# Optimization experiments

Measured on AMD Instinct MI355X. Metric: run time of the kernel, lower is better.

The kernel has to match this reference:

```python
import jax, jax.numpy as jnp
import numpy as np

NUE, NAP, E = 512, 1024, 524288
D, OC, HID, PH = 4, 64, 32, 4  # raw feat dim, out_channels, out//2, power hid


def _lin(key, fi, fo):
    k1, k2 = jax.random.split(key)
    s = 1.0 / np.sqrt(fi)
    W = jax.random.uniform(k1, (fi, fo), minval=-s, maxval=s, dtype=jnp.float32)
    b = jax.random.uniform(k2, (fo,), minval=-s, maxval=s, dtype=jnp.float32)
    return W, b


_LAYER_SPECS = [
    ("c1_msg", D + D, HID), ("c1_upd", HID + D, OC - D), ("c1_ew", 3 * D, OC - D),
    ("c2_msg", OC + D, HID), ("c2_upd", HID + D, OC - D), ("c2_ew", D + OC + D, OC - D),
    ("c3u_msg", 2 * OC, HID), ("c3u_upd", HID + OC, OC - D), ("c3u_ew", 3 * OC, OC - D),
    ("c3d_msg", 2 * OC, HID), ("c3d_upd", HID + OC, OC - D), ("c3d_ew", 3 * OC, OC - D),
    ("pe1", OC, PH), ("pe2", PH, 1),
]


def setup_inputs() -> dict:
    key = jax.random.key(0)
    ks = jax.random.split(key, 24)
    inp = {}
    inp["x_ue"] = jax.random.normal(ks[0], (NUE, D), dtype=jnp.float32)
    inp["x_ap"] = jax.random.normal(ks[1], (NAP, D), dtype=jnp.float32)
    inp["ea_up"] = jax.random.normal(ks[2], (E, D), dtype=jnp.float32)
    inp["ea_down"] = jax.random.normal(ks[3], (E, D), dtype=jnp.float32)
    inp["ei_up_src"] = jax.random.randint(ks[4], (E,), 0, NUE, dtype=jnp.int32)
    inp["ei_up_dst"] = jax.random.randint(ks[5], (E,), 0, NAP, dtype=jnp.int32)
    inp["ei_down_src"] = jax.random.randint(ks[6], (E,), 0, NAP, dtype=jnp.int32)
    inp["ei_down_dst"] = jax.random.randint(ks[7], (E,), 0, NUE, dtype=jnp.int32)
    for i, (n, fi, fo) in enumerate(_LAYER_SPECS):
        W, b = _lin(ks[8 + i], fi, fo)
        inp[n + "_W"] = W
        inp[n + "_b"] = b
    inp["pe_ln_g"] = jnp.ones((PH,), dtype=jnp.float32)
    inp["pe_ln_b"] = jnp.zeros((PH,), dtype=jnp.float32)
    return inp


def _lrelu(x):
    return jnp.where(x >= 0, x, 0.1 * x)


def _mlp1(x, W, b):  # one MLP block: Linear -> LeakyReLU(0.1) (dropout = eval identity)
    return _lrelu(x @ W + b)


def _conv_step(x_src, x_dst, ea, src_idx, dst_idx, n_dst,
               msg_W, msg_b, upd_W, upd_b, ew_W, ew_b, residual):
    xj = x_src[src_idx]                                   # [E, d_src] gather
    m = _mlp1(jnp.concatenate([xj, ea], axis=1), msg_W, msg_b)  # [E, HID]
    agg = jax.ops.segment_sum(m, dst_idx, num_segments=n_dst)   # scatter-add -> [n_dst, HID]
    tmp = _mlp1(jnp.concatenate([x_dst, agg], axis=1), upd_W, upd_b)  # [n_dst, OC-D]
    if residual:
        tmp = tmp + x_dst[:, D:]
    new_x_dst = jnp.concatenate([x_dst[:, :D], tmp], axis=1)     # [n_dst, OC]
    xi = x_dst[dst_idx]                                   # old x_dst per torch code
    e = _mlp1(jnp.concatenate([xj, ea, xi], axis=1), ew_W, ew_b)  # [E, OC-D]
    new_ea = jnp.concatenate([ea[:, :D], e], axis=1)             # [E, OC]
    return new_x_dst, new_ea


def _layernorm(x, g, b, eps=1e-5):
    mu = jnp.mean(x, axis=-1, keepdims=True)
    var = jnp.mean(jnp.square(x - mu), axis=-1, keepdims=True)
    return (x - mu) * jax.lax.rsqrt(var + eps) * g + b


def reference(x_ue, x_ap, ea_up, ea_down,
              ei_up_src, ei_up_dst, ei_down_src, ei_down_dst,
              c1_msg_W, c1_msg_b, c1_upd_W, c1_upd_b, c1_ew_W, c1_ew_b,
              c2_msg_W, c2_msg_b, c2_upd_W, c2_upd_b, c2_ew_W, c2_ew_b,
              c3u_msg_W, c3u_msg_b, c3u_upd_W, c3u_upd_b, c3u_ew_W, c3u_ew_b,
              c3d_msg_W, c3d_msg_b, c3d_upd_W, c3d_upd_b, c3d_ew_W, c3d_ew_b,
              pe1_W, pe1_b, pe2_W, pe2_b, pe_ln_g, pe_ln_b):
    # conv1: UE --up--> AP
    x_ap, ea_up = _conv_step(x_ue, x_ap, ea_up, ei_up_src, ei_up_dst, NAP,
                             c1_msg_W, c1_msg_b, c1_upd_W, c1_upd_b, c1_ew_W, c1_ew_b, False)
    # conv2: AP --down--> UE
    x_ue, ea_down = _conv_step(x_ap, x_ue, ea_down, ei_down_src, ei_down_dst, NUE,
                               c2_msg_W, c2_msg_b, c2_upd_W, c2_upd_b, c2_ew_W, c2_ew_b, False)
    # conv3 handles both edge types (residual since src_dim == out_channels)
    x_ap, ea_up = _conv_step(x_ue, x_ap, ea_up, ei_up_src, ei_up_dst, NAP,
                             c3u_msg_W, c3u_msg_b, c3u_upd_W, c3u_upd_b, c3u_ew_W, c3u_ew_b, True)
    x_ue, ea_down = _conv_step(x_ap, x_ue, ea_down, ei_down_src, ei_down_dst, NUE,
                               c3d_msg_W, c3d_msg_b, c3d_upd_W, c3d_upd_b, c3d_ew_W, c3d_ew_b, True)
    # power head on down edges: Lin -> LayerNorm -> LeakyReLU -> Lin
    h = _lrelu(_layernorm(ea_down @ pe1_W + pe1_b, pe_ln_g, pe_ln_b))
    power = h @ pe2_W + pe2_b                                   # [E, 1]
    ea_down = jnp.concatenate([ea_down[:, :D], power], axis=1)  # [E, D+1]
    return (x_ue, x_ap, ea_up, ea_down)
```

## Files before the change

kernel.cpp:

```cpp
#include <hip/hip_runtime.h>

typedef __attribute__((ext_vector_type(8))) short bf16x8;
typedef __attribute__((ext_vector_type(4))) float f32x4;

static constexpr int EN   = 524288;
static constexpr int NUE_ = 512;
static constexpr int NAP_ = 1024;
static constexpr int HID_ = 32;
static constexpr int OD_  = 60;
static constexpr int OC_  = 64;
static constexpr int NB_  = 256;
static constexpr int CH_  = EN / NB_;

__device__ __forceinline__ unsigned short f2bf(float x) {
  unsigned int u = __float_as_uint(x);
  return (unsigned short)((u + 0x7fffu + ((u >> 16) & 1u)) >> 16);
}
__device__ __forceinline__ float bf2f(unsigned int u) {
  return __uint_as_float(u << 16);
}

__global__ __launch_bounds__(256)
void lhist2x(const int* __restrict__ up_dst, const int* __restrict__ dn_dst,
             int* __restrict__ bh_up, int* __restrict__ bh_dn,
             unsigned short* __restrict__ lr_up, unsigned short* __restrict__ lr_dn,
             const float* __restrict__ c3u_ew, const float* __restrict__ c3u_msg,
             const float* __restrict__ c3d_ew, const float* __restrict__ c3d_msg,
             unsigned short* __restrict__ we3u, unsigned short* __restrict__ wm3u,
             unsigned short* __restrict__ we3d, unsigned short* __restrict__ wm3d,
             const float* __restrict__ x_ue, const float* __restrict__ x_ap,
             const float* __restrict__ c1_ew, const float* __restrict__ c1_msg,
             const float* __restrict__ c1_ew_b, const float* __restrict__ c1_msg_b,
             const float* __restrict__ c2_ew, const float* __restrict__ c2_ew_b,
             float* __restrict__ Y1j, float* __restrict__ Y1i,
             float* __restrict__ Y1m, float* __restrict__ Y2i)
{
  __shared__ int h[NAP_];
  const int t = threadIdx.x;
  if (blockIdx.x >= 2 * NB_) {
    const int xb = blockIdx.x - 2 * NB_;
    if (xb < 48) {
      const float* W; unsigned short* out; int NREAL, NPAD, i;
      if (xb < 16)      { W = c3u_ew;  out = we3u; NREAL = 60; NPAD = 64; i = xb * 256 + t; }
      else if (xb < 24) { W = c3u_msg; out = wm3u; NREAL = 32; NPAD = 32; i = (xb - 16) * 256 + t; }
      else if (xb < 40) { W = c3d_ew;  out = we3d; NREAL = 60; NPAD = 64; i = (xb - 24) * 256 + t; }
      else              { W = c3d_msg; out = wm3d; NREAL = 32; NPAD = 32; i = (xb - 40) * 256 + t; }
      if (i >= NPAD * 64) return;
      int n = i >> 6, k = i & 63;
      float v = (n < NREAL) ? W[(size_t)(64 + k) * NREAL + n] : 0.f;
      out[i] = f2bf(v);
    } else {
      const int tid = (xb - 48) * 256 + t;
      if (tid < NUE_) {
        const float4 x = *reinterpret_cast<const float4*>(x_ue + (size_t)tid * 4);
        const float xv[4] = {x.x, x.y, x.z, x.w};
        for (int o = 0; o < OD_; ++o) {
          float a = 0.f, bb = c2_ew_b[o];
          #pragma unroll
          for (int k = 0; k < 4; ++k) {
            a = fmaf(xv[k], c1_ew[k * OD_ + o], a);
            bb = fmaf(xv[k], c2_ew[(68 + k) * OD_ + o], bb);
          }
          Y1j[(size_t)tid * OD_ + o] = a;
          Y2i[(size_t)tid * OD_ + o] = bb;
        }
        for (int o = 0; o < HID_; ++o) {
          float m = c1_msg_b[o];
          #pragma unroll
          for (int k = 0; k < 4; ++k) m = fmaf(xv[k], c1_msg[k * HID_ + o], m);
          Y1m[(size_t)tid * HID_ + o] = m;
        }
      } else if (tid < NUE_ + NAP_) {
        const int r = tid - NUE_;
        const float4 x = *reinterpret_cast<const float4*>(x_ap + (size_t)r * 4);
        const float xv[4] = {x.x, x.y, x.z, x.w};
        for (int o = 0; o < OD_; ++o) {
          float a = c1_ew_b[o];
          #pragma unroll
          for (int k = 0; k < 4; ++k) a = fmaf(xv[k], c1_ew[(8 + k) * OD_ + o], a);
          Y1i[(size_t)r * OD_ + o] = a;
        }
      }
    }
    return;
  }
  const bool up = blockIdx.x < NB_;
  const int b = up ? blockIdx.x : blockIdx.x - NB_;
  const int NBINS = up ? NAP_ : NUE_;
  const int* dst = up ? up_dst : dn_dst;
  int* bh = up ? bh_up : bh_dn;
  unsigned short* lrank = up ? lr_up : lr_dn;
  for (int i = t; i < NBINS; i += 256) h[i] = 0;
  __syncthreads();
  const int base = b * CH_;
  #pragma unroll 1
  for (int i = t; i < CH_; i += 256)
    lrank[base + i] = (unsigned short)atomicAdd(&h[dst[base + i]], 1);
  __syncthreads();
  for (int i = t; i < NBINS; i += 256)
    bh[(size_t)i * NB_ + b] = h[i];
}

__global__ __launch_bounds__(64)
void bscanA2(int* __restrict__ bh_up, int* __restrict__ bh_dn,
             int* __restrict__ bs_up, int* __restrict__ bs_dn)
{
  const bool up = blockIdx.x < NAP_;
  const int bin = up ? blockIdx.x : blockIdx.x - NAP_;
  int* bh = up ? bh_up : bh_dn;
  int* binsum = up ? bs_up : bs_dn;
  const int l = threadIdx.x;
  int4 v = *reinterpret_cast<int4*>(&bh[(size_t)bin * NB_ + l * 4]);
  const int s0 = v.x, s1 = s0 + v.y, s2 = s1 + v.z, s3 = s2 + v.w;
  int inc = s3;
  #pragma unroll
  for (int d2 = 1; d2 < 64; d2 <<= 1) {
    int n = __shfl_up(inc, d2, 64);
    if (l >= d2) inc += n;
  }
  const int exc = inc - s3;
  int4 o; o.x = exc; o.y = exc + s0; o.z = exc + s1; o.w = exc + s2;
  *reinterpret_cast<int4*>(&bh[(size_t)bin * NB_ + l * 4]) = o;
  if (l == 63) binsum[bin] = inc;
}

__global__ __launch_bounds__(256)
void bscanB2(const int* __restrict__ bs_up, int* __restrict__ off_up,
             const int* __restrict__ bs_dn, int* __restrict__ off_dn)
{
  const bool up = blockIdx.x == 0;
  const int NBINS = up ? NAP_ : NUE_;
  const int K = NBINS / 256;
  const int* binsum = up ? bs_up : bs_dn;
  int* off = up ? off_up : off_dn;
  __shared__ int wtot[4];
  const int t = threadIdx.x, lane = t & 63, wid = t >> 6;
  int loc[4]; int s = 0;
  for (int k = 0; k < K; ++k) { loc[k] = binsum[t * K + k]; s += loc[k]; }
  int inc = s;
  #pragma unroll
  for (int d2 = 1; d2 < 64; d2 <<= 1) {
    int n = __shfl_up(inc, d2, 64);
    if (lane >= d2) inc += n;
  }
  if (lane == 63) wtot[wid] = inc;
  __syncthreads();
  int woff = 0;
  #pragma unroll
  for (int ww = 0; ww < 4; ++ww) if (ww < wid) woff += wtot[ww];
  int a = woff + inc - s;
  for (int k = 0; k < K; ++k) { off[t * K + k] = a; a += loc[k]; }
  if (t == 255) off[NBINS] = a;
}

__global__ __launch_bounds__(256)
void rankc2(const int* __restrict__ up_dst, const int* __restrict__ up_src,
            const int* __restrict__ dn_dst, const int* __restrict__ dn_src,
            const unsigned short* __restrict__ lr_up, const unsigned short* __restrict__ lr_dn,
            const int* __restrict__ bh_up, const int* __restrict__ bh_dn,
            const int* __restrict__ off_up, const int* __restrict__ off_dn,
            int* __restrict__ rank_dn,
            int* __restrict__ perm_up, int* __restrict__ srcP_up, int* __restrict__ dstP_up,
            int* __restrict__ perm_dn, int* __restrict__ srcP_dn, int* __restrict__ dstP_dn)
{
  const int gid = blockIdx.x * 256 + threadIdx.x;
  const bool up = gid < EN;
  const int e = up ? gid : gid - EN;
  const int* dst = up ? up_dst : dn_dst;
  const int* src = up ? up_src : dn_src;
  const unsigned short* lrank = up ? lr_up : lr_dn;
  const int* bh = up ? bh_up : bh_dn;
  const int* off = up ? off_up : off_dn;
  const int blk = e / CH_;
  const int d = dst[e];
  const int rk = off[d] + bh[(size_t)d * NB_ + blk] + (int)lrank[e];
  if (up) {
    perm_up[rk] = e; srcP_up[rk] = src[e]; dstP_up[rk] = d;
  } else {
    rank_dn[e] = rk;
    perm_dn[rk] = e; srcP_dn[rk] = src[e]; dstP_dn[rk] = d;
  }
}

__global__ __launch_bounds__(256)
void e12n(const float* __restrict__ ea_in,
          const int* __restrict__ perm, const int* __restrict__ srcP,
          const int* __restrict__ off,
          const float* __restrict__ Yje, const float* __restrict__ Yie,
          const float* __restrict__ Ym,
          const float* __restrict__ We,
          const float* __restrict__ Wm,
          unsigned short* __restrict__ outB,
          const float* __restrict__ x_in,
          const float* __restrict__ W, const float* __restrict__ b,
          float* __restrict__ x_out,
          const float* __restrict__ WtA, float* __restrict__ YA,
          const float* __restrict__ WtB, const float* __restrict__ bB, float* __restrict__ YB,
          const float* __restrict__ WtC, const float* __restrict__ bC, float* __restrict__ YC)
{
  __shared__ unsigned short Eb[64 * 72];
  __shared__ float RedF[64][33];
  __shared__ float Part[8][33];
  __shared__ float Ag[32];
  __shared__ float Xr[4];
  __shared__ float Xn[OC_];
  const int d = blockIdx.x, t = threadIdx.x;
  const int beg = off[d], end = off[d + 1];
  const int r = t >> 2, j = t & 3;
  const int c0 = j * 15, m0 = j * 8;
  if (t < 4) Xr[t] = x_in[(size_t)d * 4 + t];
  float yie[15];
  #pragma unroll
  for (int c = 0; c < 15; ++c) yie[c] = Yie[(size_t)d * OD_ + c0 + c];
  float am[8] = {0.f, 0.f, 0.f, 0.f, 0.f, 0.f, 0.f, 0.f};

  for (int sb = beg; sb < end; sb += 64) {
    const int slot = sb + r;
    const bool act = slot < end;
    const int e = act ? perm[slot] : 0;
    const int s = act ? srcP[slot] : 0;
    float4 ea = act ? *reinterpret_cast<const float4*>(ea_in + (size_t)e * 4)
                    : make_float4(0.f, 0.f, 0.f, 0.f);
    const float eav[4] = {ea.x, ea.y, ea.z, ea.w};
    float acc[15];
    #pragma unroll
    for (int c = 0; c < 15; ++c) acc[c] = Yje[(size_t)s * OD_ + c0 + c] + yie[c];
    #pragma unroll
    for (int k = 0; k < 4; ++k)
      #pragma unroll
      for (int c = 0; c < 15; ++c)
        acc[c] = fmaf(eav[k], We[k * OD_ + c0 + c], acc[c]);
    if (act) {
      #pragma unroll
      for (int c = 0; c < 15; ++c) {
        float v = acc[c] >= 0.f ? acc[c] : 0.1f * acc[c];
        Eb[r * 72 + 4 + c0 + c] = f2bf(v);
      }
      if (j == 0) {
        Eb[r * 72 + 0] = f2bf(ea.x); Eb[r * 72 + 1] = f2bf(ea.y);
        Eb[r * 72 + 2] = f2bf(ea.z); Eb[r * 72 + 3] = f2bf(ea.w);
      }
    }
    float m[8];
    #pragma unroll
    for (int c = 0; c < 8; ++c) m[c] = Ym[(size_t)s * HID_ + m0 + c];
    #pragma unroll
    for (int k = 0; k < 4; ++k)
      #pragma unroll
      for (int c = 0; c < 8; ++c)
        m[c] = fmaf(eav[k], Wm[k * HID_ + m0 + c], m[c]);
    if (act) {
      #pragma unroll
      for (int c = 0; c < 8; ++c)
        am[c] += m[c] >= 0.f ? m[c] : 0.1f * m[c];
    }
    __syncthreads();
    const int nact = end - sb < 64 ? end - sb : 64;
    for (int idx = t; idx < nact * 8; idx += 256) {
      int row = idx >> 3, ch = idx & 7;
      *reinterpret_cast<uint4*>(outB + (size_t)(sb + row) * OC_ + ch * 8) =
          *reinterpret_cast<const uint4*>(&Eb[row * 72 + ch * 8]);
    }
    __syncthreads();
  }
  #pragma unroll
  for (int c = 0; c < 8; ++c) RedF[r][m0 + c] = am[c];
  __syncthreads();
  {
    const int col = t & 31, g = t >> 5;
    float s = 0.f;
    #pragma unroll
    for (int r2 = 0; r2 < 8; ++r2) s += RedF[g * 8 + r2][col];
    Part[g][col] = s;
  }
  __syncthreads();
  if (t < 32) {
    float s = 0.f;
    #pragma unroll
    for (int g2 = 0; g2 < 8; ++g2) s += Part[g2][t];
    Ag[t] = s;
  }
  __syncthreads();
  if (t < OD_) {
    float acc = b[t];
    #pragma unroll
    for (int k = 0; k < 4; ++k) acc = fmaf(Xr[k], W[k * OD_ + t], acc);
    #pragma unroll 4
    for (int k = 0; k < HID_; ++k) acc = fmaf(Ag[k], W[(4 + k) * OD_ + t], acc);
    acc = acc >= 0.f ? acc : 0.1f * acc;
    x_out[(size_t)d * OC_ + 4 + t] = acc;
    Xn[4 + t] = acc;
  } else if (t < OC_) {
    x_out[(size_t)d * OC_ + (t - OD_)] = Xr[t - OD_];
    Xn[t - OD_] = Xr[t - OD_];
  }
  __syncthreads();
  if (t < OD_) {
    float a = 0.f;
    #pragma unroll 4
    for (int k = 0; k < OC_; ++k) a = fmaf(Xn[k], WtA[k * OD_ + t], a);
    YA[(size_t)d * OD_ + t] = a;
  } else if (t >= 64 && t < 96) {
    const int cc = t - 64;
    float a = bB[cc];
    #pragma unroll 4
    for (int k = 0; k < OC_; ++k) a = fmaf(Xn[k], WtB[k * HID_ + cc], a);
    YB[(size_t)d * HID_ + cc] = a;
  } else if (t >= 128 && t < 188) {
    const int cc = t - 128;
    float a = bC[cc];
    #pragma unroll 4
    for (int k = 0; k < OC_; ++k) a = fmaf(Xn[k], WtC[k * OD_ + cc], a);
    YC[(size_t)d * OD_ + cc] = a;
  }
}

template<bool FUSE>
__global__ __launch_bounds__(256)
void edge3(const unsigned short* __restrict__ eaB,
           const float* __restrict__ ea0_src,
           const int* __restrict__ perm,
           const int* __restrict__ srcP, const int* __restrict__ dstP,
           const unsigned short* __restrict__ Wet, const unsigned short* __restrict__ Wmt,
           const float* __restrict__ Yje, const float* __restrict__ Yie,
           const float* __restrict__ Ym,
           float* __restrict__ agg,
           float* __restrict__ ea_out,
           float* __restrict__ pT,
           const float* __restrict__ pe1_W)
{
  const int t = threadIdx.x, l = t & 63, w = t >> 6;
  const int lr = l & 15, lkb = l >> 4;
  const int sW = blockIdx.x * 256 + w * 64;

  bf16x8 be[4][2], bm[2][2];
  #pragma unroll
  for (int nt = 0; nt < 4; ++nt)
    #pragma unroll
    for (int kk = 0; kk < 2; ++kk)
      be[nt][kk] = *reinterpret_cast<const bf16x8*>(Wet + (nt * 16 + lr) * 64 + kk * 32 + lkb * 8);
  #pragma unroll
  for (int nt = 0; nt < 2; ++nt)
    #pragma unroll
    for (int kk = 0; kk < 2; ++kk)
      bm[nt][kk] = *reinterpret_cast<const bf16x8*>(Wmt + (nt * 16 + lr) * 64 + kk * 32 + lkb * 8);

  float accLo = 0.f, accHi = 0.f;
  int curD = -1;

  #pragma unroll 1
  for (int tile = 0; tile < 4; ++tile) {
    const int s0t = sW + tile * 16;
    const unsigned short* ar = eaB + (size_t)(s0t + lr) * OC_ + lkb * 8;
    bf16x8 a[2];
    a[0] = *reinterpret_cast<const bf16x8*>(ar);
    a[1] = *reinterpret_cast<const bf16x8*>(ar + 32);

    f32x4 accE[4] = {f32x4{0,0,0,0}, f32x4{0,0,0,0}, f32x4{0,0,0,0}, f32x4{0,0,0,0}};
    f32x4 accM[2] = {f32x4{0,0,0,0}, f32x4{0,0,0,0}};
    #pragma unroll
    for (int kk = 0; kk < 2; ++kk) {
      #pragma unroll
      for (int nt = 0; nt < 4; ++nt)
        accE[nt] = __builtin_amdgcn_mfma_f32_16x16x32_bf16(a[kk], be[nt][kk], accE[nt], 0, 0, 0);
      #pragma unroll
      for (int nt = 0; nt < 2; ++nt)
        accM[nt] = __builtin_amdgcn_mfma_f32_16x16x32_bf16(a[kk], bm[nt][kk], accM[nt], 0, 0, 0);
    }
    #pragma unroll
    for (int r = 0; r < 4; ++r) {
      const int sl = s0t + lkb * 4 + r;
      const int s = srcP[sl], d = dstP[sl];
      float v0 = accM[0][r] + Ym[(size_t)s * HID_ + lr];
      float v1 = accM[1][r] + Ym[(size_t)s * HID_ + 16 + lr];
      v0 = v0 >= 0.f ? v0 : 0.1f * v0;
      v1 = v1 >= 0.f ? v1 : 0.1f * v1;
      const int q0 = (2 * lr) & 15, q1 = (2 * lr + 1) & 15;
      float t00 = __shfl(v0, q0, 16), t10 = __shfl(v1, q0, 16);
      float t01 = __shfl(v0, q1, 16), t11 = __shfl(v1, q1, 16);
      float lo = (lr < 8) ? t00 : t10;
      float hi = (lr < 8) ? t01 : t11;
      if (d != curD) {
        if (curD >= 0) {
          atomicAdd(&agg[(size_t)curD * HID_ + 2 * lr], accLo);
          atomicAdd(&agg[(size_t)curD * HID_ + 2 * lr + 1], accHi);
        }
        curD = d; accLo = lo; accHi = hi;
      } else {
        accLo += lo; accHi += hi;
      }

      float val[4];
      #pragma unroll
      for (int nt = 0; nt < 4; ++nt) {
        int col = nt * 16 + lr;
        float v = (col < OD_)
            ? accE[nt][r] + Yje[(size_t)s * OD_ + col] + Yie[(size_t)d * OD_ + col]
            : 0.f;
        val[nt] = v >= 0.f ? v : 0.1f * v;
      }
      if constexpr (!FUSE) {
        const int e = perm[sl];
        #pragma unroll
        for (int nt = 0; nt < 4; ++nt) {
          int col = nt * 16 + lr;
          if (col < OD_) ea_out[(size_t)e * OC_ + 4 + col] = val[nt];
        }
        if (lr == 0) {
          float4 ea0 = *reinterpret_cast<const float4*>(ea0_src + (size_t)e * 4);
          *reinterpret_cast<float4*>(ea_out + (size_t)e * OC_) = ea0;
        }
      } else {
        float p4[4] = {0.f, 0.f, 0.f, 0.f};
        #pragma unroll
        for (int nt = 0; nt < 4; ++nt) {
          int col = nt * 16 + lr;
          if (col < OD_) {
            #pragma unroll
            for (int jj = 0; jj < 4; ++jj)
              p4[jj] = fmaf(val[nt], pe1_W[(4 + col) * 4 + jj], p4[jj]);
          }
        }
        #pragma unroll
        for (int mk = 1; mk < 16; mk <<= 1) {
          #pragma unroll
          for (int jj = 0; jj < 4; ++jj)
            p4[jj] += __shfl_xor(p4[jj], mk, 64);
        }
        if (lr == 0)
          *reinterpret_cast<float4*>(pT + (size_t)sl * 4) =
              make_float4(p4[0], p4[1], p4[2], p4[3]);
      }
    }
  }
  if (curD >= 0) {
    atomicAdd(&agg[(size_t)curD * HID_ + 2 * lr], accLo);
    atomicAdd(&agg[(size_t)curD * HID_ + 2 * lr + 1], accHi);
  }
}

template<int LX, bool RES>
__device__ __forceinline__
void nodeup_body(int d, int t,
                 const float* __restrict__ x_in,
                 const float* __restrict__ agg,
                 const float* __restrict__ W, const float* __restrict__ b,
                 float* __restrict__ x_out,
                 const float* WtA, float* YA,
                 const float* WtB, const float* bB, float* YB)
{
  __shared__ float Ag[32];
  __shared__ float Xr[LX];
  __shared__ float Xn[OC_];
  if (t < 32) Ag[t] = agg[(size_t)d * HID_ + t];
  if (t < LX) Xr[t] = x_in[(size_t)d * LX + t];
  __syncthreads();
  if (t < OD_) {
    float acc = b[t];
    #pragma unroll 4
    for (int k = 0; k < LX; ++k) acc = fmaf(Xr[k], W[k * OD_ + t], acc);
    #pragma unroll 4
    for (int k = 0; k < HID_; ++k) acc = fmaf(Ag[k], W[(LX + k) * OD_ + t], acc);
    acc = acc >= 0.f ? acc : 0.1f * acc;
    if constexpr (RES) acc += Xr[4 + t];
    x_out[(size_t)d * OC_ + 4 + t] = acc;
    Xn[4 + t] = acc;
  } else if (t < OC_) {
    x_out[(size_t)d * OC_ + (t - OD_)] = Xr[t - OD_];
    Xn[t - OD_] = Xr[t - OD_];
  }
  if (WtA == nullptr) return;
  __syncthreads();
  if (t < OD_) {
    float a = 0.f;
    #pragma unroll 4
    for (int k = 0; k < OC_; ++k) a = fmaf(Xn[k], WtA[k * OD_ + t], a);
    YA[(size_t)d * OD_ + t] = a;
  } else if (t >= 64 && t < 96) {
    const int cc = t - 64;
    float a = bB[cc];
    #pragma unroll 4
    for (int k = 0; k < OC_; ++k) a = fmaf(Xn[k], WtB[k * HID_ + cc], a);
    YB[(size_t)d * HID_ + cc] = a;
  }
}

template<int LX, bool RES>
__global__ __launch_bounds__(256)
void nodeupT(const float* __restrict__ x_in, const float* __restrict__ agg,
             const float* __restrict__ W, const float* __restrict__ b,
             float* __restrict__ x_out,
             const float* WtA, float* YA,
             const float* WtB, const float* bB, float* YB)
{
  nodeup_body<LX, RES>(blockIdx.x, threadIdx.x, x_in, agg, W, b, x_out,
                       WtA, YA, WtB, bB, YB);
}

__global__ __launch_bounds__(256)
void nodeup_pow(const float* __restrict__ x_in, const float* __restrict__ agg,
                const float* __restrict__ W, const float* __restrict__ b,
                float* __restrict__ x_out,
                const float* __restrict__ ea0_src, const int* __restrict__ rank,
                const float* __restrict__ pT,
                const float* __restrict__ pe1_W, const float* __restrict__ pe1_b,
                const float* __restrict__ pe2_W, const float* __restrict__ pe2_b,
                const float* __restrict__ ln_g, const float* __restrict__ ln_b,
                float* __restrict__ outp)
{
  if (blockIdx.x < NUE_) {
    nodeup_body<OC_, true>(blockIdx.x, threadIdx.x, x_in, agg, W, b, x_out,
                           nullptr, nullptr, nullptr, nullptr, nullptr);
    return;
  }
  const int e = (blockIdx.x - NUE_) * 256 + threadIdx.x;
  const int rk = rank[e];
  const float4 p4 = *reinterpret_cast<const float4*>(pT + (size_t)rk * 4);
  const float4 ea0 = *reinterpret_cast<const float4*>(ea0_src + (size_t)e * 4);
  const float pv[4] = {p4.x, p4.y, p4.z, p4.w};
  float v4[4];
  #pragma unroll
  for (int jj = 0; jj < 4; ++jj)
    v4[jj] = pv[jj] + pe1_b[jj]
           + ea0.x * pe1_W[0 * 4 + jj] + ea0.y * pe1_W[1 * 4 + jj]
           + ea0.z * pe1_W[2 * 4 + jj] + ea0.w * pe1_W[3 * 4 + jj];
  const float mu = 0.25f * (v4[0] + v4[1] + v4[2] + v4[3]);
  float var = 0.f;
  #pragma unroll
  for (int jj = 0; jj < 4; ++jj) { float dd = v4[jj] - mu; var = fmaf(dd, dd, var); }
  var *= 0.25f;
  const float rstd = rsqrtf(var + 1e-5f);
  float p = pe2_b[0];
  #pragma unroll
  for (int jj = 0; jj < 4; ++jj) {
    float h = (v4[jj] - mu) * rstd * ln_g[jj] + ln_b[jj];
    h = h >= 0.f ? h : 0.1f * h;
    p = fmaf(h, pe2_W[jj], p);
  }
  float* orow = outp + (size_t)e * 5;
  orow[0] = ea0.x; orow[1] = ea0.y; orow[2] = ea0.z; orow[3] = ea0.w;
  orow[4] = p;
}

extern "C" void kernel_launch(void* const* d_in, const int* in_sizes, int n_in,
                              void* d_out, int out_size, void* d_ws, size_t ws_size,
                              hipStream_t stream)
{
  const float* x_ue    = (const float*)d_in[0];
  const float* x_ap    = (const float*)d_in[1];
  const float* ea_up   = (const float*)d_in[2];
  const float* ea_down = (const float*)d_in[3];
  const int* up_src = (const int*)d_in[4];
  const int* up_dst = (const int*)d_in[5];
  const int* dn_src = (const int*)d_in[6];
  const int* dn_dst = (const int*)d_in[7];
  const float* c1_msg_W = (const float*)d_in[8];  const float* c1_msg_b = (const float*)d_in[9];
  const float* c1_upd_W = (const float*)d_in[10]; const float* c1_upd_b = (const float*)d_in[11];
  const float* c1_ew_W  = (const float*)d_in[12]; const float* c1_ew_b  = (const float*)d_in[13];
  const float* c2_msg_W = (const float*)d_in[14]; const float* c2_msg_b = (const float*)d_in[15];
  const float* c2_upd_W = (const float*)d_in[16]; const float* c2_upd_b = (const float*)d_in[17];
  const float* c2_ew_W  = (const float*)d_in[18]; const float* c2_ew_b  = (const float*)d_in[19];
  const float* c3u_msg_W= (const float*)d_in[20]; const float* c3u_msg_b= (const float*)d_in[21];
  const float* c3u_upd_W= (const float*)d_in[22]; const float* c3u_upd_b= (const float*)d_in[23];
  const float* c3u_ew_W = (const float*)d_in[24]; const float* c3u_ew_b = (const float*)d_in[25];
  const float* c3d_msg_W= (const float*)d_in[26]; const float* c3d_msg_b= (const float*)d_in[27];
  const float* c3d_upd_W= (const float*)d_in[28]; const float* c3d_upd_b= (const float*)d_in[29];
  const float* c3d_ew_W = (const float*)d_in[30]; const float* c3d_ew_b = (const float*)d_in[31];
  const float* pe1_W = (const float*)d_in[32]; const float* pe1_b = (const float*)d_in[33];
  const float* pe2_W = (const float*)d_in[34]; const float* pe2_b = (const float*)d_in[35];
  const float* ln_g  = (const float*)d_in[36]; const float* ln_b  = (const float*)d_in[37];

  float* out    = (float*)d_out;
  float* x_ue_o = out;
  float* x_ap_o = out + (size_t)NUE_ * OC_;
  float* ea_up_o = x_ap_o + (size_t)NAP_ * OC_;
  float* ea_dn_o = ea_up_o + (size_t)EN * OC_;

  float* agg3 = (float*)d_ws;
  float* agg4 = agg3 + NAP_ * HID_;
  int* ip = (int*)(agg4 + NUE_ * HID_);
  int* rank_dn = ip; ip += EN;
  int* perm_up = ip; ip += EN;
  int* src_upP = ip; ip += EN;
  int* dst_upP = ip; ip += EN;
  int* perm_dn = ip; ip += EN;
  int* src_dnP = ip; ip += EN;
  int* dst_dnP = ip; ip += EN;
  int* bh_up   = ip; ip += NAP_ * NB_;
  int* bh_dn   = ip; ip += NUE_ * NB_;
  int* off_up  = ip; ip += NAP_ + 1;
  int* off_dn  = ip; ip += NUE_ + 1;
  int* bs_up   = ip; ip += NAP_;
  int* bs_dn   = ip; ip += NUE_;
  unsigned short* lr_up = (unsigned short*)ip; ip += EN / 2;
  unsigned short* lr_dn = (unsigned short*)ip; ip += EN / 2;
  float* p = (float*)ip;
  float* Y1j = p;  p += NUE_ * OD_;  float* Y1i = p; p += NAP_ * OD_;  float* Y1m = p; p += NUE_ * HID_;
  float* Y2j = p;  p += NAP_ * OD_;  float* Y2i = p; p += NUE_ * OD_;  float* Y2m = p; p += NAP_ * HID_;
  float* Y3uj = p; p += NUE_ * OD_;  float* Y3ui = p; p += NAP_ * OD_; float* Y3um = p; p += NUE_ * HID_;
  float* Y3dj = p; p += NAP_ * OD_;  float* Y3di = p; p += NUE_ * OD_; float* Y3dm = p; p += NAP_ * HID_;
  float* pT = p;   p += (size_t)EN * 4;
  unsigned short* us = (unsigned short*)p;
  unsigned short* ea_up_bf = us;  us += (size_t)EN * OC_;
  unsigned short* ea_dn_bf = us;  us += (size_t)EN * OC_;
  unsigned short* we3u = us; us += 64 * 64;
  unsigned short* wm3u = us; us += 32 * 64;
  unsigned short* we3d = us; us += 64 * 64;
  unsigned short* wm3d = us; us += 32 * 64;

  hipMemsetAsync(agg3, 0, sizeof(float) * (NAP_ + NUE_) * HID_, stream);

  const dim3 blk(256);
  const dim3 ege(EN / 256);

  lhist2x<<<dim3(2 * NB_ + 56), blk, 0, stream>>>(
      up_dst, dn_dst, bh_up, bh_dn, lr_up, lr_dn,
      c3u_ew_W, c3u_msg_W, c3d_ew_W, c3d_msg_W, we3u, wm3u, we3d, wm3d,
      x_ue, x_ap, c1_ew_W, c1_msg_W, c1_ew_b, c1_msg_b, c2_ew_W, c2_ew_b,
      Y1j, Y1i, Y1m, Y2i);
  bscanA2<<<dim3(NAP_ + NUE_), dim3(64), 0, stream>>>(bh_up, bh_dn, bs_up, bs_dn);
  bscanB2<<<dim3(2), blk, 0, stream>>>(bs_up, off_up, bs_dn, off_dn);
  rankc2<<<dim3(2 * EN / 256), blk, 0, stream>>>(
      up_dst, up_src, dn_dst, dn_src, lr_up, lr_dn, bh_up, bh_dn, off_up, off_dn,
      rank_dn, perm_up, src_upP, dst_upP, perm_dn, src_dnP, dst_dnP);

  e12n<<<dim3(NAP_), blk, 0, stream>>>(
      ea_up, perm_up, src_upP, off_up, Y1j, Y1i, Y1m,
      c1_ew_W + 4 * OD_, c1_msg_W + 4 * HID_, ea_up_bf,
      x_ap, c1_upd_W, c1_upd_b, x_ap_o,
      c2_ew_W, Y2j, c2_msg_W, c2_msg_b, Y2m,
      c3u_ew_W + 128 * OD_, c3u_ew_b, Y3ui);

  e12n<<<dim3(NUE_), blk, 0, stream>>>(
      ea_down, perm_dn, src_dnP, off_dn, Y2j, Y2i, Y2m,
      c2_ew_W + 64 * OD_, c2_msg_W + 64 * HID_, ea_dn_bf,
      x_ue, c2_upd_W, c2_upd_b, x_ue_o,
      c3u_ew_W, Y3uj, c3u_msg_W, c3u_msg_b, Y3um,
      c3d_ew_W + 128 * OD_, c3d_ew_b, Y3di);

  edge3<false><<<ege, blk, 0, stream>>>(
      ea_up_bf, ea_up, perm_up, src_upP, dst_upP, we3u, wm3u,
      Y3uj, Y3ui, Y3um, agg3, ea_up_o, nullptr, nullptr);
  nodeupT<64, true><<<dim3(NAP_), blk, 0, stream>>>(
      x_ap_o, agg3, c3u_upd_W, c3u_upd_b, x_ap_o,
      c3d_ew_W, Y3dj, c3d_msg_W, c3d_msg_b, Y3dm);

  edge3<true><<<ege, blk, 0, stream>>>(
      ea_dn_bf, nullptr, nullptr, src_dnP, dst_dnP, we3d, wm3d,
      Y3dj, Y3di, Y3dm, agg4, nullptr, pT, pe1_W);
  nodeup_pow<<<dim3(NUE_ + EN / 256), blk, 0, stream>>>(
      x_ue_o, agg4, c3d_upd_W, c3d_upd_b, x_ue_o,
      ea_down, rank_dn, pT, pe1_W, pe1_b, pe2_W, pe2_b, ln_g, ln_b, ea_dn_o);
}
```

Measured before the change: 434.0 us.

## Split per-node edge kernels across multiple blocks and move node update out

The conv1/conv2 edge kernels previously ran one block per destination node: 1024 blocks for the up direction and 512 for the down direction, each looping over about 512 or 1024 edges. They now split each node's edge segment across 2 or 4 blocks and combine partial message sums with atomicAdd into a zeroed aggregation buffer. The node-update and precompute work that used to follow in the same kernel moves into separate nodeupT launches, which gain an optional third projection. This raises parallelism on a GPU with many CUs, at the cost of extra launches, atomics and a larger memset. The edge3 tile loop unroll also changes from 1 to 2.

```diff
diff --git a/kernel.cpp b/kernel.cpp
--- a/kernel.cpp
+++ b/kernel.cpp
@@ -182,33 +182,30 @@
   }
 }
 
+template<int S>
 __global__ __launch_bounds__(256)
-void e12n(const float* __restrict__ ea_in,
-          const int* __restrict__ perm, const int* __restrict__ srcP,
-          const int* __restrict__ off,
-          const float* __restrict__ Yje, const float* __restrict__ Yie,
-          const float* __restrict__ Ym,
-          const float* __restrict__ We,
-          const float* __restrict__ Wm,
-          unsigned short* __restrict__ outB,
-          const float* __restrict__ x_in,
-          const float* __restrict__ W, const float* __restrict__ b,
-          float* __restrict__ x_out,
-          const float* __restrict__ WtA, float* __restrict__ YA,
-          const float* __restrict__ WtB, const float* __restrict__ bB, float* __restrict__ YB,
-          const float* __restrict__ WtC, const float* __restrict__ bC, float* __restrict__ YC)
+void e12nS(const float* __restrict__ ea_in,
+           const int* __restrict__ perm, const int* __restrict__ srcP,
+           const int* __restrict__ off,
+           const float* __restrict__ Yje, const float* __restrict__ Yie,
+           const float* __restrict__ Ym,
+           const float* __restrict__ We,
+           const float* __restrict__ Wm,
+           unsigned short* __restrict__ outB,
+           float* __restrict__ agg)
 {
   __shared__ unsigned short Eb[64 * 72];
   __shared__ float RedF[64][33];
   __shared__ float Part[8][33];
-  __shared__ float Ag[32];
-  __shared__ float Xr[4];
-  __shared__ float Xn[OC_];
-  const int d = blockIdx.x, t = threadIdx.x;
-  const int beg = off[d], end = off[d + 1];
+  const int d = blockIdx.x / S, part = blockIdx.x % S;
+  const int t = threadIdx.x;
+  const int beg0 = off[d], end0 = off[d + 1];
+  const int len = end0 - beg0;
+  const int chunk = (len + S - 1) / S;
+  const int beg = beg0 + part * chunk;
+  const int end = (beg + chunk < end0) ? (beg + chunk) : end0;
   const int r = t >> 2, j = t & 3;
   const int c0 = j * 15, m0 = j * 8;
-  if (t < 4) Xr[t] = x_in[(size_t)d * 4 + t];
   float yie[15];
   #pragma unroll
   for (int c = 0; c < 15; ++c) yie[c] = Yie[(size_t)d * OD_ + c0 + c];
@@ -278,40 +275,7 @@
     float s = 0.f;
     #pragma unroll
     for (int g2 = 0; g2 < 8; ++g2) s += Part[g2][t];
-    Ag[t] = s;
-  }
-  __syncthreads();
-  if (t < OD_) {
-    float acc = b[t];
-    #pragma unroll
-    for (int k = 0; k < 4; ++k) acc = fmaf(Xr[k], W[k * OD_ + t], acc);
-    #pragma unroll 4
-    for (int k = 0; k < HID_; ++k) acc = fmaf(Ag[k], W[(4 + k) * OD_ + t], acc);
-    acc = acc >= 0.f ? acc : 0.1f * acc;
-    x_out[(size_t)d * OC_ + 4 + t] = acc;
-    Xn[4 + t] = acc;
-  } else if (t < OC_) {
-    x_out[(size_t)d * OC_ + (t - OD_)] = Xr[t - OD_];
-    Xn[t - OD_] = Xr[t - OD_];
-  }
-  __syncthreads();
-  if (t < OD_) {
-    float a = 0.f;
-    #pragma unroll 4
-    for (int k = 0; k < OC_; ++k) a = fmaf(Xn[k], WtA[k * OD_ + t], a);
-    YA[(size_t)d * OD_ + t] = a;
-  } else if (t >= 64 && t < 96) {
-    const int cc = t - 64;
-    float a = bB[cc];
-    #pragma unroll 4
-    for (int k = 0; k < OC_; ++k) a = fmaf(Xn[k], WtB[k * HID_ + cc], a);
-    YB[(size_t)d * HID_ + cc] = a;
-  } else if (t >= 128 && t < 188) {
-    const int cc = t - 128;
-    float a = bC[cc];
-    #pragma unroll 4
-    for (int k = 0; k < OC_; ++k) a = fmaf(Xn[k], WtC[k * OD_ + cc], a);
-    YC[(size_t)d * OD_ + cc] = a;
+    atomicAdd(&agg[(size_t)d * HID_ + t], s);
   }
 }
 
@@ -348,7 +312,7 @@
   float accLo = 0.f, accHi = 0.f;
   int curD = -1;
 
-  #pragma unroll 1
+  #pragma unroll 2
   for (int tile = 0; tile < 4; ++tile) {
     const int s0t = sW + tile * 16;
     const unsigned short* ar = eaB + (size_t)(s0t + lr) * OC_ + lkb * 8;
@@ -447,7 +411,8 @@
                  const float* __restrict__ W, const float* __restrict__ b,
                  float* __restrict__ x_out,
                  const float* WtA, float* YA,
-                 const float* WtB, const float* bB, float* YB)
+                 const float* WtB, const float* bB, float* YB,
+                 const float* WtC, const float* bC, float* YC)
 {
   __shared__ float Ag[32];
   __shared__ float Xr[LX];
@@ -482,6 +447,12 @@
     #pragma unroll 4
     for (int k = 0; k < OC_; ++k) a = fmaf(Xn[k], WtB[k * HID_ + cc], a);
     YB[(size_t)d * HID_ + cc] = a;
+  } else if (WtC != nullptr && t >= 128 && t < 188) {
+    const int cc = t - 128;
+    float a = bC[cc];
+    #pragma unroll 4
+    for (int k = 0; k < OC_; ++k) a = fmaf(Xn[k], WtC[k * OD_ + cc], a);
+    YC[(size_t)d * OD_ + cc] = a;
   }
 }
 
@@ -491,10 +462,11 @@
              const float* __restrict__ W, const float* __restrict__ b,
              float* __restrict__ x_out,
              const float* WtA, float* YA,
-             const float* WtB, const float* bB, float* YB)
+             const float* WtB, const float* bB, float* YB,
+             const float* WtC, const float* bC, float* YC)
 {
   nodeup_body<LX, RES>(blockIdx.x, threadIdx.x, x_in, agg, W, b, x_out,
-                       WtA, YA, WtB, bB, YB);
+                       WtA, YA, WtB, bB, YB, WtC, bC, YC);
 }
 
 __global__ __launch_bounds__(256)
@@ -510,7 +482,8 @@
 {
   if (blockIdx.x < NUE_) {
     nodeup_body<OC_, true>(blockIdx.x, threadIdx.x, x_in, agg, W, b, x_out,
-                           nullptr, nullptr, nullptr, nullptr, nullptr);
+                           nullptr, nullptr, nullptr, nullptr, nullptr,
+                           nullptr, nullptr, nullptr);
     return;
   }
   const int e = (blockIdx.x - NUE_) * 256 + threadIdx.x;
@@ -576,7 +549,9 @@
   float* ea_up_o = x_ap_o + (size_t)NAP_ * OC_;
   float* ea_dn_o = ea_up_o + (size_t)EN * OC_;
 
-  float* agg3 = (float*)d_ws;
+  float* agg1 = (float*)d_ws;
+  float* agg2 = agg1 + NAP_ * HID_;
+  float* agg3 = agg2 + NUE_ * HID_;
   float* agg4 = agg3 + NAP_ * HID_;
   int* ip = (int*)(agg4 + NUE_ * HID_);
   int* rank_dn = ip; ip += EN;
@@ -608,7 +583,7 @@
   unsigned short* we3d = us; us += 64 * 64;
   unsigned short* wm3d = us; us += 32 * 64;
 
-  hipMemsetAsync(agg3, 0, sizeof(float) * (NAP_ + NUE_) * HID_, stream);
+  hipMemsetAsync(agg1, 0, sizeof(float) * (NAP_ + NUE_) * 2 * HID_, stream);
 
   const dim3 blk(256);
   const dim3 ege(EN / 256);
@@ -624,17 +599,19 @@
       up_dst, up_src, dn_dst, dn_src, lr_up, lr_dn, bh_up, bh_dn, off_up, off_dn,
       rank_dn, perm_up, src_upP, dst_upP, perm_dn, src_dnP, dst_dnP);
 
-  e12n<<<dim3(NAP_), blk, 0, stream>>>(
+  e12nS<2><<<dim3(NAP_ * 2), blk, 0, stream>>>(
       ea_up, perm_up, src_upP, off_up, Y1j, Y1i, Y1m,
-      c1_ew_W + 4 * OD_, c1_msg_W + 4 * HID_, ea_up_bf,
-      x_ap, c1_upd_W, c1_upd_b, x_ap_o,
+      c1_ew_W + 4 * OD_, c1_msg_W + 4 * HID_, ea_up_bf, agg1);
+  nodeupT<4, false><<<dim3(NAP_), blk, 0, stream>>>(
+      x_ap, agg1, c1_upd_W, c1_upd_b, x_ap_o,
       c2_ew_W, Y2j, c2_msg_W, c2_msg_b, Y2m,
       c3u_ew_W + 128 * OD_, c3u_ew_b, Y3ui);
 
-  e12n<<<dim3(NUE_), blk, 0, stream>>>(
+  e12nS<4><<<dim3(NUE_ * 4), blk, 0, stream>>>(
       ea_down, perm_dn, src_dnP, off_dn, Y2j, Y2i, Y2m,
-      c2_ew_W + 64 * OD_, c2_msg_W + 64 * HID_, ea_dn_bf,
-      x_ue, c2_upd_W, c2_upd_b, x_ue_o,
+      c2_ew_W + 64 * OD_, c2_msg_W + 64 * HID_, ea_dn_bf, agg2);
+  nodeupT<4, false><<<dim3(NUE_), blk, 0, stream>>>(
+      x_ue, agg2, c2_upd_W, c2_upd_b, x_ue_o,
       c3u_ew_W, Y3uj, c3u_msg_W, c3u_msg_b, Y3um,
       c3d_ew_W + 128 * OD_, c3d_ew_b, Y3di);
 
@@ -643,7 +620,8 @@
       Y3uj, Y3ui, Y3um, agg3, ea_up_o, nullptr, nullptr);
   nodeupT<64, true><<<dim3(NAP_), blk, 0, stream>>>(
       x_ap_o, agg3, c3u_upd_W, c3u_upd_b, x_ap_o,
-      c3d_ew_W, Y3dj, c3d_msg_W, c3d_msg_b, Y3dm);
+      c3d_ew_W, Y3dj, c3d_msg_W, c3d_msg_b, Y3dm,
+      nullptr, nullptr, nullptr);
 
   edge3<true><<<ege, blk, 0, stream>>>(
       ea_dn_bf, nullptr, nullptr, src_dnP, dst_dnP, we3d, wm3d,
```

Result: slower. 443.2 us (+2.1%).
